# Kernel tuning notes

Measured on AMD Instinct MI355X. Metric: run time of the kernel, lower is better.

Reference implementation:

```python
import jax, jax.numpy as jnp
import numpy as np

NEG_INF = -1e30

def _pool_unpool(x, k):
    # x: [B, C, H, W]. Non-overlapping max pool with window k (floor-mode,
    # matching torch MaxPool2d default), then MaxUnpool: scatter the pooled max
    # back to its argmax location within each window, zeros elsewhere.
    B, C, H, W = x.shape
    Hc, Wc = (H // k) * k, (W // k) * k  # cropped region covered by windows
    xc = x[:, :, :Hc, :Wc]
    # reshape into windows: [B, C, H/k, k, W/k, k] -> [B, C, H/k, W/k, k*k]
    xw = xc.reshape(B, C, Hc // k, k, Wc // k, k).transpose(0, 1, 2, 4, 3, 5)
    xw = xw.reshape(B, C, Hc // k, Wc // k, k * k)
    mx = jnp.max(xw, axis=-1, keepdims=True)
    am = jnp.argmax(xw, axis=-1)  # first max index, matches torch tie-breaking
    onehot = (jnp.arange(k * k) == am[..., None])
    yw = jnp.where(onehot, mx, jnp.zeros_like(mx))
    yc = yw.reshape(B, C, Hc // k, Wc // k, k, k).transpose(0, 1, 2, 4, 3, 5)
    yc = yc.reshape(B, C, Hc, Wc)
    # output_size=size in torch unpool -> pad uncovered border with zeros
    return jnp.pad(yc, ((0, 0), (0, 0), (0, H - Hc), (0, W - Wc)))

def setup_inputs() -> dict:
    key = jax.random.key(0)
    x = jax.random.uniform(key, (16, 1, 1080, 1920), dtype=jnp.float32)
    return {"x": x}

def reference(x):
    k = 3
    x = _pool_unpool(x, k)
    x = _pool_unpool(x, k + 2)
    x = _pool_unpool(x, k + 3)
    return x
```

## Files before the change

kernel.cpp:

```cpp
#include <hip/hip_runtime.h>


#define IMG_H 1080
#define IMG_W 1920
#define NT 256

__global__ __launch_bounds__(NT) void pooling_nms_kernel(
    const float* __restrict__ x, float* __restrict__ out) {
    __shared__ float comp[4][900];
    __shared__ float sv[4][100];
    __shared__ int   sp[4][100];
    __shared__ float w5v[4][36];
    __shared__ int   w5p[4][36];

    const int t = threadIdx.x;
    const int w = t >> 6;
    const int ln = t & 63;

    const int stc = blockIdx.x * 4 + w;
    const int str = blockIdx.y;
    const size_t base = (size_t)blockIdx.z * ((size_t)IMG_H * IMG_W) +
                        (size_t)str * 30 * IMG_W + (size_t)stc * 30;
    const float* src = x + base;
    float* dst = out + base;

    float4* c4 = reinterpret_cast<float4*>(comp[w]);
    for (int i = ln; i < 225; i += 64) c4[i] = make_float4(0.f, 0.f, 0.f, 0.f);

#pragma unroll
    for (int b = 0; b < 2; ++b) {
        const int win = b * 64 + ln;
        if (win < 100) {
            const int wr = win / 10, wc = win - wr * 10;
            const float* p = src + (size_t)(wr * 3) * IMG_W + wc * 3;
            float mx = -1.0f;
            int am = 0;
#pragma unroll
            for (int r = 0; r < 3; ++r) {
                const float v0 = p[(size_t)r * IMG_W + 0];
                const float v1 = p[(size_t)r * IMG_W + 1];
                const float v2 = p[(size_t)r * IMG_W + 2];
                const int rr = wr * 3 + r, cc = wc * 3;
                if (v0 > mx) { mx = v0; am = (rr << 5) | cc; }
                if (v1 > mx) { mx = v1; am = (rr << 5) | (cc + 1); }
                if (v2 > mx) { mx = v2; am = (rr << 5) | (cc + 2); }
            }
            sv[w][win] = mx;
            sp[w][win] = am;
        }
    }
    __syncthreads();

    if (ln < 36) {
        const int a = ln / 6, b = ln - (ln / 6) * 6;
        const int rlo = (5 * a) / 3, rhi = (5 * a + 4) / 3;
        const int clo = (5 * b) / 3, chi = (5 * b + 4) / 3;
        float bv = -1.0f;
        int bp = 0x7FFFFFFF;
        for (int r3 = rlo; r3 <= rhi; ++r3)
            for (int c3 = clo; c3 <= chi; ++c3) {
                const int idx = r3 * 10 + c3;
                const float v = sv[w][idx];
                const int p = sp[w][idx];
                const int r = p >> 5, c = p & 31;
                const bool in =
                    ((unsigned)(r - 5 * a) < 5u) & ((unsigned)(c - 5 * b) < 5u);
                if (in && (v > bv || (v == bv && p < bp))) { bv = v; bp = p; }
            }
        w5v[w][ln] = bv;
        w5p[w][ln] = bp;
    }
    __syncthreads();

    if (ln < 25) {
        const int a = ln / 5, b = ln - (ln / 5) * 5;
        const int rlo = (6 * a) / 5, clo = (6 * b) / 5;
        float bv = -1.0f;
        int bp = 0x7FFFFFFF;
#pragma unroll
        for (int dr = 0; dr < 2; ++dr)
#pragma unroll
            for (int dc = 0; dc < 2; ++dc) {
                const int idx = (rlo + dr) * 6 + (clo + dc);
                const float v = w5v[w][idx];
                const int p = w5p[w][idx];
                const int r = p >> 5, c = p & 31;
                const bool in = (v >= 0.0f) &
                                ((unsigned)(r - 6 * a) < 6u) &
                                ((unsigned)(c - 6 * b) < 6u);
                if (in && (v > bv || (v == bv && p < bp))) { bv = v; bp = p; }
            }
        if (bv >= 0.0f) comp[w][(bp >> 5) * 30 + (bp & 31)] = bv;
    }
    __syncthreads();

    const float2* c2 = reinterpret_cast<const float2*>(comp[w]);
    for (int i = ln; i < 450; i += 64) {
        const int r = i / 15, cc = i - r * 15;
        *reinterpret_cast<float2*>(dst + (size_t)r * IMG_W + cc * 2) = c2[i];
    }
}

extern "C" void kernel_launch(void* const* d_in, const int* in_sizes, int n_in,
                              void* d_out, int out_size, void* d_ws, size_t ws_size,
                              hipStream_t stream) {
    const float* x = (const float*)d_in[0];
    float* out = (float*)d_out;
    dim3 grid(IMG_W / 120, IMG_H / 30, 16);
    pooling_nms_kernel<<<grid, NT, 0, stream>>>(x, out);
}
```

Measured before the change: 249.5 us.

## Make waves persistent over several tiles with register prefetch and wave barriers

```diff
diff --git a/kernel.cpp b/kernel.cpp
--- a/kernel.cpp
+++ b/kernel.cpp
@@ -1,103 +1,171 @@
 #include <hip/hip_runtime.h>
 
 
-#define IMG_H 1080
-#define IMG_W 1920
+#define H 1080
+#define W 1920
 #define NT 256
+#define NBLK 1536
+#define TPW 6
 
-__global__ __launch_bounds__(NT) void pooling_nms_kernel(
+__global__ __launch_bounds__(NT, 6) void pooling_nms_kernel(
     const float* __restrict__ x, float* __restrict__ out) {
-    __shared__ float comp[4][900];
     __shared__ float sv[4][100];
     __shared__ int   sp[4][100];
     __shared__ float w5v[4][36];
     __shared__ int   w5p[4][36];
+    __shared__ float comp[4][900];
 
     const int t = threadIdx.x;
     const int w = t >> 6;
     const int ln = t & 63;
 
-    const int stc = blockIdx.x * 4 + w;
-    const int str = blockIdx.y;
-    const size_t base = (size_t)blockIdx.z * ((size_t)IMG_H * IMG_W) +
-                        (size_t)str * 30 * IMG_W + (size_t)stc * 30;
-    const float* src = x + base;
-    float* dst = out + base;
+    const int wr0 = ln / 10, wc0 = ln - wr0 * 10;
+    const int wn1 = 64 + ln;
+    const int wr1 = wn1 / 10, wc1 = wn1 - wr1 * 10;
+    const long off0 = (long)(wr0 * 3) * W + wc0 * 3;
+    const long off1 = (long)(wr1 * 3) * W + wc1 * 3;
+    const int sr = ln / 15, sc = ln - sr * 15;
+    const int p2a = ln / 6, p2b = ln - p2a * 6;
+    const int rlo2 = (5 * p2a) / 3, rhi2 = (5 * p2a + 4) / 3;
+    const int clo2 = (5 * p2b) / 3, chi2 = (5 * p2b + 4) / 3;
+    const int p3a = ln / 5, p3b = ln - p3a * 5;
+    const int rlo3 = (6 * p3a) / 5, clo3 = (6 * p3b) / 5;
 
-    float4* c4 = reinterpret_cast<float4*>(comp[w]);
-    for (int i = ln; i < 225; i += 64) c4[i] = make_float4(0.f, 0.f, 0.f, 0.f);
+    const int wid = blockIdx.x * 4 + w;
+    int s = wid * TPW;
 
+    auto base_of = [&](int ss) -> size_t {
+        const int str = ss >> 6, stc = ss & 63;
+        const int b = str / 36, r30 = str - b * 36;
+        return (size_t)b * ((size_t)H * W) + (size_t)(r30 * 30) * W +
+               (size_t)stc * 30;
+    };
+
+    size_t base = base_of(s);
+    float va[9], vb[9];
+    {
+        const float* p0 = x + base + off0;
 #pragma unroll
-    for (int b = 0; b < 2; ++b) {
-        const int win = b * 64 + ln;
-        if (win < 100) {
-            const int wr = win / 10, wc = win - wr * 10;
-            const float* p = src + (size_t)(wr * 3) * IMG_W + wc * 3;
-            float mx = -1.0f;
-            int am = 0;
+        for (int r = 0; r < 3; ++r) {
+            va[r * 3 + 0] = p0[(size_t)r * W + 0];
+            va[r * 3 + 1] = p0[(size_t)r * W + 1];
+            va[r * 3 + 2] = p0[(size_t)r * W + 2];
+        }
+        if (ln < 36) {
+            const float* p1 = x + base + off1;
 #pragma unroll
             for (int r = 0; r < 3; ++r) {
-                const float v0 = p[(size_t)r * IMG_W + 0];
-                const float v1 = p[(size_t)r * IMG_W + 1];
-                const float v2 = p[(size_t)r * IMG_W + 2];
-                const int rr = wr * 3 + r, cc = wc * 3;
-                if (v0 > mx) { mx = v0; am = (rr << 5) | cc; }
-                if (v1 > mx) { mx = v1; am = (rr << 5) | (cc + 1); }
-                if (v2 > mx) { mx = v2; am = (rr << 5) | (cc + 2); }
+                vb[r * 3 + 0] = p1[(size_t)r * W + 0];
+                vb[r * 3 + 1] = p1[(size_t)r * W + 1];
+                vb[r * 3 + 2] = p1[(size_t)r * W + 2];
             }
-            sv[w][win] = mx;
-            sp[w][win] = am;
         }
     }
-    __syncthreads();
 
-    if (ln < 36) {
-        const int a = ln / 6, b = ln - (ln / 6) * 6;
-        const int rlo = (5 * a) / 3, rhi = (5 * a + 4) / 3;
-        const int clo = (5 * b) / 3, chi = (5 * b + 4) / 3;
-        float bv = -1.0f;
-        int bp = 0x7FFFFFFF;
-        for (int r3 = rlo; r3 <= rhi; ++r3)
-            for (int c3 = clo; c3 <= chi; ++c3) {
-                const int idx = r3 * 10 + c3;
-                const float v = sv[w][idx];
-                const int p = sp[w][idx];
-                const int r = p >> 5, c = p & 31;
-                const bool in =
-                    ((unsigned)(r - 5 * a) < 5u) & ((unsigned)(c - 5 * b) < 5u);
-                if (in && (v > bv || (v == bv && p < bp))) { bv = v; bp = p; }
+    for (int j = 0; j < TPW; ++j) {
+        const size_t curbase = base;
+
+        {
+            float mx = -1.0f; int am = 0;
+#pragma unroll
+            for (int r = 0; r < 3; ++r)
+#pragma unroll
+                for (int c = 0; c < 3; ++c) {
+                    const float v = va[r * 3 + c];
+                    if (v > mx) { mx = v; am = ((wr0 * 3 + r) << 5) | (wc0 * 3 + c); }
+                }
+            sv[w][ln] = mx; sp[w][ln] = am;
+            if (ln < 36) {
+                mx = -1.0f; am = 0;
+#pragma unroll
+                for (int r = 0; r < 3; ++r)
+#pragma unroll
+                    for (int c = 0; c < 3; ++c) {
+                        const float v = vb[r * 3 + c];
+                        if (v > mx) { mx = v; am = ((wr1 * 3 + r) << 5) | (wc1 * 3 + c); }
+                    }
+                sv[w][wn1] = mx; sp[w][wn1] = am;
             }
-        w5v[w][ln] = bv;
-        w5p[w][ln] = bp;
-    }
-    __syncthreads();
+        }
 
-    if (ln < 25) {
-        const int a = ln / 5, b = ln - (ln / 5) * 5;
-        const int rlo = (6 * a) / 5, clo = (6 * b) / 5;
-        float bv = -1.0f;
-        int bp = 0x7FFFFFFF;
+        if (j + 1 < TPW) {
+            ++s;
+            base = base_of(s);
+            const float* p0 = x + base + off0;
 #pragma unroll
-        for (int dr = 0; dr < 2; ++dr)
+            for (int r = 0; r < 3; ++r) {
+                va[r * 3 + 0] = p0[(size_t)r * W + 0];
+                va[r * 3 + 1] = p0[(size_t)r * W + 1];
+                va[r * 3 + 2] = p0[(size_t)r * W + 2];
+            }
+            if (ln < 36) {
+                const float* p1 = x + base + off1;
 #pragma unroll
-            for (int dc = 0; dc < 2; ++dc) {
-                const int idx = (rlo + dr) * 6 + (clo + dc);
-                const float v = w5v[w][idx];
-                const int p = w5p[w][idx];
-                const int r = p >> 5, c = p & 31;
-                const bool in = (v >= 0.0f) &
-                                ((unsigned)(r - 6 * a) < 6u) &
-                                ((unsigned)(c - 6 * b) < 6u);
-                if (in && (v > bv || (v == bv && p < bp))) { bv = v; bp = p; }
+                for (int r = 0; r < 3; ++r) {
+                    vb[r * 3 + 0] = p1[(size_t)r * W + 0];
+                    vb[r * 3 + 1] = p1[(size_t)r * W + 1];
+                    vb[r * 3 + 2] = p1[(size_t)r * W + 2];
+                }
             }
-        if (bv >= 0.0f) comp[w][(bp >> 5) * 30 + (bp & 31)] = bv;
-    }
-    __syncthreads();
+        }
+        __builtin_amdgcn_wave_barrier();
 
-    const float2* c2 = reinterpret_cast<const float2*>(comp[w]);
-    for (int i = ln; i < 450; i += 64) {
-        const int r = i / 15, cc = i - r * 15;
-        *reinterpret_cast<float2*>(dst + (size_t)r * IMG_W + cc * 2) = c2[i];
+        if (ln < 36) {
+            float bv = -1.0f; int bp = 0x7FFFFFFF;
+            for (int r3 = rlo2; r3 <= rhi2; ++r3)
+                for (int c3 = clo2; c3 <= chi2; ++c3) {
+                    const int idx = r3 * 10 + c3;
+                    const float v = sv[w][idx];
+                    const int p = sp[w][idx];
+                    const int r = p >> 5, c = p & 31;
+                    const bool in = ((unsigned)(r - 5 * p2a) < 5u) &
+                                    ((unsigned)(c - 5 * p2b) < 5u);
+                    if (in && (v > bv || (v == bv && p < bp))) { bv = v; bp = p; }
+                }
+            w5v[w][ln] = bv;
+            w5p[w][ln] = bp;
+        }
+        __builtin_amdgcn_wave_barrier();
+
+        float4* c4 = reinterpret_cast<float4*>(comp[w]);
+#pragma unroll
+        for (int k2 = 0; k2 < 4; ++k2) {
+            const int i = ln + 64 * k2;
+            if (i < 225) c4[i] = make_float4(0.f, 0.f, 0.f, 0.f);
+        }
+
+        if (ln < 25) {
+            float bv = -1.0f; int bp = 0x7FFFFFFF;
+#pragma unroll
+            for (int dr = 0; dr < 2; ++dr)
+#pragma unroll
+                for (int dc = 0; dc < 2; ++dc) {
+                    const int idx = (rlo3 + dr) * 6 + (clo3 + dc);
+                    const float v = w5v[w][idx];
+                    const int p = w5p[w][idx];
+                    const int r = p >> 5, c = p & 31;
+                    const bool in = (v >= 0.0f) &
+                                    ((unsigned)(r - 6 * p3a) < 6u) &
+                                    ((unsigned)(c - 6 * p3b) < 6u);
+                    if (in && (v > bv || (v == bv && p < bp))) { bv = v; bp = p; }
+                }
+            if (bv >= 0.0f) comp[w][(bp >> 5) * 30 + (bp & 31)] = bv;
+        }
+        __builtin_amdgcn_wave_barrier();
+
+        if (ln < 60) {
+            float* d = out + curbase + (size_t)sr * W + sc * 2;
+            const float* cb = &comp[w][sr * 30 + sc * 2];
+#pragma unroll
+            for (int k2 = 0; k2 < 8; ++k2) {
+                const int r = sr + 4 * k2;
+                if (r < 30) {
+                    const float2 v2 = *reinterpret_cast<const float2*>(cb + 120 * k2);
+                    *reinterpret_cast<float2*>(d + (size_t)(4 * k2) * W) = v2;
+                }
+            }
+        }
+        __builtin_amdgcn_wave_barrier();
     }
 }
 
@@ -106,6 +174,5 @@
                               hipStream_t stream) {
     const float* x = (const float*)d_in[0];
     float* out = (float*)d_out;
-    dim3 grid(IMG_W / 120, IMG_H / 30, 16);
-    pooling_nms_kernel<<<grid, NT, 0, stream>>>(x, out);
+    pooling_nms_kernel<<<dim3(NBLK, 1, 1), NT, 0, stream>>>(x, out);
 }
```

Measured after the change: 313.2 us. 1.26x slower.
